# Performance work log

Measured on AMD Instinct MI355X. Metric: run time of the kernel, lower is better.

## Reference

```python
import jax, jax.numpy as jnp
import numpy as np

SEQ = 2048
D_MODEL = 4096
N_HEADS = 16
D_HEAD = D_MODEL // N_HEADS
D_FF = 4 * D_MODEL


def setup_inputs() -> dict:
    key = jax.random.key(0)
    ks = jax.random.split(key, 8)
    s = 0.02
    return {
        "x": jax.random.normal(ks[0], (SEQ, D_MODEL), jnp.float32),
        "attn_bias": jax.random.normal(ks[1], (1, SEQ, SEQ), jnp.float32) * 0.1,
        "ln_scale": jnp.ones((D_MODEL,), jnp.float32),
        "ln_offset": jnp.zeros((D_MODEL,), jnp.float32),
        "wq": jax.random.normal(ks[2], (D_MODEL, D_MODEL), jnp.float32) * s,
        "wk": jax.random.normal(ks[3], (D_MODEL, D_MODEL), jnp.float32) * s,
        "wv": jax.random.normal(ks[4], (D_MODEL, D_MODEL), jnp.float32) * s,
        "wo": jax.random.normal(ks[5], (D_MODEL, D_MODEL), jnp.float32) * s,
        "w_ffn": jax.random.normal(ks[6], (D_MODEL, D_FF), jnp.float32) * s,
        "b_ffn": jnp.zeros((D_FF,), jnp.float32),
        "w_ffn_o": jax.random.normal(ks[7], (D_FF, D_MODEL), jnp.float32) * s,
        "b_ffn_o": jnp.zeros((D_MODEL,), jnp.float32),
    }


def reference(x, attn_bias, ln_scale, ln_offset, wq, wk, wv, wo,
              w_ffn, b_ffn, w_ffn_o, b_ffn_o):
    # ReplicatedLayerNorm (single shard: f_psum is identity)
    mean = jnp.mean(x, axis=-1, keepdims=True)
    var = jnp.var(x, axis=-1, keepdims=True)
    h = ln_scale * jax.lax.rsqrt(var + 1e-5) * (x - mean) + ln_offset

    seq = h.shape[0]
    q = (h @ wq).reshape(seq, N_HEADS, D_HEAD)
    k = (h @ wk).reshape(seq, N_HEADS, D_HEAD)
    v = (h @ wv).reshape(seq, N_HEADS, D_HEAD)

    logits = jnp.einsum('thd,Thd->htT', q, k) / np.float32(np.sqrt(D_HEAD))
    causal = jnp.tril(jnp.ones((seq, seq), jnp.float32))
    logits = logits - 1e10 * (1.0 - causal)
    logits = logits + attn_bias
    weights = jax.nn.softmax(logits, axis=-1)
    attn_vec = jnp.einsum('htT,Thd->thd', weights, v).reshape(seq, D_MODEL)
    attn_out = attn_vec @ wo

    # parallel GELU MLP on the same normed input
    ff = jax.nn.gelu(h @ w_ffn + b_ffn)
    dense_out = ff @ w_ffn_o + b_ffn_o

    return attn_out + dense_out
```

## Files before the change

kernel.cpp:

```cpp
#include <hip/hip_runtime.h>
#include <stdint.h>

#define SEQ 2048
#define DM 4096
#define NHEADS 16
#define DHEAD 256
#define DFF 16384

typedef __attribute__((ext_vector_type(8))) short short8;
typedef __attribute__((ext_vector_type(4))) float f32x4;
typedef __attribute__((ext_vector_type(4))) float float4v;
typedef __attribute__((ext_vector_type(4))) unsigned short ushort4v;
typedef __attribute__((ext_vector_type(8))) unsigned short ushort8v;

__device__ __forceinline__ unsigned short f2b(float f) {
    uint32_t u = __builtin_bit_cast(uint32_t, f);
    u = (u + 0x7FFFu + ((u >> 16) & 1u)) >> 16;
    return (unsigned short)u;
}

__device__ __forceinline__ void gload_lds16(const void* g, void* l) {
    __builtin_amdgcn_global_load_lds((const __attribute__((address_space(1))) void*)g,
                                     (__attribute__((address_space(3))) void*)l, 16, 0, 0);
}

__global__ __launch_bounds__(256) void transpose_all(
    const float* __restrict__ wq, const float* __restrict__ wk, const float* __restrict__ wv,
    const float* __restrict__ wo, const float* __restrict__ wf1, const float* __restrict__ wf2,
    unsigned short* __restrict__ dqkv, unsigned short* __restrict__ dwo,
    unsigned short* __restrict__ df1, unsigned short* __restrict__ df2) {
    int b = blockIdx.x;
    const float* src;
    unsigned short* dst;
    int ldS, ldD, tx;
    if (b < 12288) {
        int w = b >> 12;
        b &= 4095;
        src = (w == 0) ? wq : (w == 1) ? wk : wv;
        dst = dqkv + (size_t)w * DM * DM;
        ldS = DM; ldD = DM; tx = 64;
    } else if (b < 16384) {
        b -= 12288; src = wo; dst = dwo; ldS = DM; ldD = DM; tx = 64;
    } else if (b < 32768) {
        b -= 16384; src = wf1; dst = df1; ldS = DFF; ldD = DM; tx = 256;
    } else {
        b -= 32768; src = wf2; dst = df2; ldS = DM; ldD = DFF; tx = 64;
    }
    const int bx = b % tx, by = b / tx;

    __shared__ unsigned short tl[64 * 66];
    int r0 = by << 6, c0 = bx << 6;
    int tid = threadIdx.x;
#pragma unroll
    for (int it = 0; it < 4; ++it) {
        int e = (tid + it * 256) * 4;
        int rr = e >> 6, cc = e & 63;
        float4v v = *(const float4v*)(src + (size_t)(r0 + rr) * ldS + c0 + cc);
#pragma unroll
        for (int j = 0; j < 4; ++j) tl[rr * 66 + cc + j] = f2b(v[j]);
    }
    __syncthreads();
#pragma unroll
    for (int it = 0; it < 2; ++it) {
        int e = tid + it * 256;
        int oc = e >> 3;
        int k8 = (e & 7) * 8;
        ushort8v w;
#pragma unroll
        for (int j = 0; j < 8; ++j) w[j] = tl[(k8 + j) * 66 + oc];
        *(ushort8v*)(dst + (size_t)(c0 + oc) * ldD + r0 + k8) = w;
    }
}

__global__ __launch_bounds__(256) void transpose_bf(const unsigned short* __restrict__ src,
                                                    unsigned short* __restrict__ dst,
                                                    int ldS, int ldD) {
    __shared__ unsigned short tl[64 * 66];
    int r0 = blockIdx.y << 6, c0 = blockIdx.x << 6;
    int tid = threadIdx.x;
#pragma unroll
    for (int it = 0; it < 4; ++it) {
        int e = (tid + it * 256) * 4;
        int rr = e >> 6, cc = e & 63;
        ushort4v v = *(const ushort4v*)(src + (size_t)(r0 + rr) * ldS + c0 + cc);
#pragma unroll
        for (int j = 0; j < 4; ++j) tl[rr * 66 + cc + j] = v[j];
    }
    __syncthreads();
#pragma unroll
    for (int it = 0; it < 2; ++it) {
        int e = tid + it * 256;
        int oc = e >> 3;
        int k8 = (e & 7) * 8;
        ushort8v w;
#pragma unroll
        for (int j = 0; j < 8; ++j) w[j] = tl[(k8 + j) * 66 + oc];
        *(ushort8v*)(dst + (size_t)(c0 + oc) * ldD + r0 + k8) = w;
    }
}

__global__ __launch_bounds__(256) void ln_kernel(const float* __restrict__ x,
                                                 const float* __restrict__ sc,
                                                 const float* __restrict__ of,
                                                 unsigned short* __restrict__ h) {
    int row = blockIdx.x;
    int tid = threadIdx.x, lane = tid & 63, wave = tid >> 6;
    const float4v* xr = (const float4v*)(x + (size_t)row * DM);
    float4v v[4];
    float s = 0.f, s2 = 0.f;
#pragma unroll
    for (int i = 0; i < 4; ++i) {
        v[i] = xr[tid + i * 256];
#pragma unroll
        for (int j = 0; j < 4; ++j) { s += v[i][j]; s2 += v[i][j] * v[i][j]; }
    }
#pragma unroll
    for (int o = 1; o < 64; o <<= 1) { s += __shfl_xor(s, o); s2 += __shfl_xor(s2, o); }
    __shared__ float rs[4], rs2[4];
    if (lane == 0) { rs[wave] = s; rs2[wave] = s2; }
    __syncthreads();
    s = rs[0] + rs[1] + rs[2] + rs[3];
    s2 = rs2[0] + rs2[1] + rs2[2] + rs2[3];
    float mean = s * (1.0f / DM);
    float var = s2 * (1.0f / DM) - mean * mean;
    float inv = rsqrtf(var + 1e-5f);
#pragma unroll
    for (int i = 0; i < 4; ++i) {
        int c = (tid + i * 256) * 4;
        ushort4v o4;
#pragma unroll
        for (int j = 0; j < 4; ++j)
            o4[j] = f2b((v[i][j] - mean) * inv * sc[c + j] + of[c + j]);
        *(ushort4v*)(h + (size_t)row * DM + c) = o4;
    }
}

#define MF(a, b, c) __builtin_amdgcn_mfma_f32_16x16x32_bf16(a, b, c, 0, 0, 0)
#define FENCE() asm volatile("" ::: "memory")
#define BARR() __builtin_amdgcn_s_barrier()

#define RDA4(BUF, MB)                                                                    \
    _Pragma("unroll") for (int i2 = 0; i2 < 4; ++i2) {                                   \
        af[(MB) + i2][0] = *(const short8*)((BUF) + (arowb + ((MB) + i2) * 16) * 64 + ca0);\
        af[(MB) + i2][1] = *(const short8*)((BUF) + (arowb + ((MB) + i2) * 16) * 64 + ca1);\
    }
#define RDB4(BUF)                                                                        \
    _Pragma("unroll") for (int j2 = 0; j2 < 4; ++j2) {                                   \
        bf[j2][0] = *(const short8*)((BUF) + (brow + j2 * 16) * 64 + ca0);               \
        bf[j2][1] = *(const short8*)((BUF) + (brow + j2 * 16) * 64 + ca1);               \
    }
#define MMQ(MB, NB)                                                                      \
    __builtin_amdgcn_s_setprio(1);                                                       \
    _Pragma("unroll") for (int kk = 0; kk < 2; ++kk)                                     \
        _Pragma("unroll") for (int i2 = 0; i2 < 4; ++i2)                                 \
            _Pragma("unroll") for (int j2 = 0; j2 < 2; ++j2)                             \
                acc[(MB) + i2][(NB) + j2] =                                              \
                    MF(af[(MB) + i2][kk], bf[(NB) + j2][kk], acc[(MB) + i2][(NB) + j2]); \
    __builtin_amdgcn_s_setprio(0)

template <int SPLIT>
__global__ __launch_bounds__(512, 1) void gemm2sq(
    int M, int nwg0,
    const unsigned short* __restrict__ A_0, int K_0, const unsigned short* __restrict__ BT_0,
    void* __restrict__ C_0, int N_0, int ldc_0, const float* __restrict__ bias_0, int epi_0,
    const unsigned short* __restrict__ A_1, int K_1, const unsigned short* __restrict__ BT_1,
    void* __restrict__ C_1, int N_1, int ldc_1, const float* __restrict__ bias_1, int epi_1) {
    __shared__ unsigned short aL[2][256 * 64];
    __shared__ unsigned short bL[2][256 * 64];

    int b = blockIdx.x;
    const unsigned short *A, *BT;
    void* Cout;
    int N, ldc, epi, Kfull;
    const float* bias;
    if (b < nwg0) {
        A = A_0; Kfull = K_0; BT = BT_0; Cout = C_0; N = N_0; ldc = ldc_0; bias = bias_0; epi = epi_0;
    } else {
        b -= nwg0;
        A = A_1; Kfull = K_1; BT = BT_1; Cout = C_1; N = N_1; ldc = ldc_1; bias = bias_1; epi = epi_1;
    }

    const int nby = M >> 8, nbx = N >> 8;
    const int nwg = nby * nbx;
    int sp = 0;
    if (SPLIT == 2) { sp = (b >= nwg) ? 1 : 0; b -= sp * nwg; }
    const int Keff = Kfull / SPLIT;
    const int koff = sp * Keff;

    const int slabw = nbx >> 3;
    const int xcd = b & 7;
    const int jj = b >> 3;
    const int bx = xcd * slabw + jj / nby;
    const int by = jj % nby;
    const int bm0 = by << 8, bn0 = bx << 8;

    const int tid = threadIdx.x, lane = tid & 63, wave = tid >> 6;
    const int wm = wave >> 2, wn = wave & 3;
    const int l15 = lane & 15, kl = lane >> 4;

    const int rh = tid >> 3;
    const int cb_s = (tid & 7) << 4;
    const int kx = (cb_s ^ ((rh & 7) << 4)) >> 1;

    const unsigned short* Abase = A + (size_t)(bm0 + rh) * Kfull + koff + kx;
    const unsigned short* Bbase = BT + (size_t)(bn0 + rh) * Kfull + koff + kx;

    auto stageA = [&](int v, int h) {
        const unsigned short* g = Abase + (size_t)v * 64 + (size_t)(h * 128) * Kfull;
        char* l = (char*)aL[v & 1] + h * 16384 + tid * 16;
        gload_lds16(g, l);
        gload_lds16(g + (size_t)64 * Kfull, l + 8192);
    };
    auto stageB = [&](int v, int h) {
        const unsigned short* g = Bbase + (size_t)v * 64 + (size_t)(h * 128) * Kfull;
        char* l = (char*)bL[v & 1] + h * 16384 + tid * 16;
        gload_lds16(g, l);
        gload_lds16(g + (size_t)64 * Kfull, l + 8192);
    };

    const int arowb = wm * 128 + l15;
    const int brow = wn * 64 + l15;
    const int sa = (l15 & 7) << 4;
    const int ca0 = ((kl * 16) ^ sa) >> 1;
    const int ca1 = ((64 + kl * 16) ^ sa) >> 1;

    f32x4 acc[8][4];
#pragma unroll
    for (int i = 0; i < 8; ++i)
#pragma unroll
        for (int j2 = 0; j2 < 4; ++j2) acc[i][j2] = (f32x4){0.f, 0.f, 0.f, 0.f};

    short8 af[8][2], bf[4][2];

    stageA(0, 0); stageA(0, 1); stageB(0, 0); stageB(0, 1); stageB(1, 0); stageB(1, 1);
    asm volatile("s_waitcnt vmcnt(4)" ::: "memory");
    BARR();

    const int NI = (Keff >> 6) >> 1;
    for (int t2 = 0; t2 < NI; ++t2) {
        const int u = t2 << 1;
        const bool last = (t2 == NI - 1);
        const unsigned short* a0 = aL[0];
        const unsigned short* b0 = bL[0];
        const unsigned short* a1 = aL[1];
        const unsigned short* b1 = bL[1];

        RDA4(a0, 0); RDB4(b0);
        stageA(u + 1, 0);
        FENCE(); BARR();
        MMQ(0, 0);
        BARR();
        RDA4(a0, 4);
        stageA(u + 1, 1);
        FENCE(); BARR();
        MMQ(0, 2);
        BARR();
        if (!last) stageB(u + 2, 0);
        FENCE(); BARR();
        MMQ(4, 0);
        BARR();
        if (!last) stageB(u + 2, 1);
        FENCE(); BARR();
        MMQ(4, 2);
        if (last) { asm volatile("s_waitcnt vmcnt(0)" ::: "memory"); }
        else      { asm volatile("s_waitcnt vmcnt(4)" ::: "memory"); }
        BARR();

        RDA4(a1, 0); RDB4(b1);
        if (!last) stageA(u + 2, 0);
        FENCE(); BARR();
        MMQ(0, 0);
        BARR();
        RDA4(a1, 4);
        if (!last) stageA(u + 2, 1);
        FENCE(); BARR();
        MMQ(0, 2);
        BARR();
        if (!last) stageB(u + 3, 0);
        FENCE(); BARR();
        MMQ(4, 0);
        BARR();
        if (!last) stageB(u + 3, 1);
        FENCE(); BARR();
        MMQ(4, 2);
        if (!last) { asm volatile("s_waitcnt vmcnt(4)" ::: "memory"); }
        BARR();
    }

    const int r0 = bm0 + wm * 128 + kl * 4;
    const int c0g = bn0 + wn * 64 + l15;
#pragma unroll
    for (int mi = 0; mi < 8; ++mi) {
#pragma unroll
        for (int nj = 0; nj < 4; ++nj) {
            int col = c0g + nj * 16;
#pragma unroll
            for (int r = 0; r < 4; ++r) {
                int row = r0 + mi * 16 + r;
                float v = acc[mi][nj][r];
                if (epi == 0) {
                    ((unsigned short*)Cout)[(size_t)row * ldc + col] = f2b(v);
                } else if (epi == 1) {
                    ((float*)Cout)[(size_t)sp * M * N + (size_t)row * ldc + col] = v;
                } else {
                    v += bias[col];
                    float z = 1.5957691216f * (v + 0.044715f * v * v * v);
                    float g = v / (1.0f + __expf(-z));
                    ((unsigned short*)Cout)[(size_t)row * ldc + col] = f2b(g);
                }
            }
        }
    }
}

__global__ __launch_bounds__(256) void final_reduce(const float* __restrict__ fp,
                                                    const float* __restrict__ wp,
                                                    const float* __restrict__ bias,
                                                    float* __restrict__ out) {
    size_t i = (size_t)blockIdx.x * 256 + threadIdx.x;
    const float4v* f0 = (const float4v*)fp;
    const float4v* f1 = (const float4v*)(fp + (size_t)SEQ * DM);
    const float4v* w0 = (const float4v*)wp;
    const float4v* w1 = (const float4v*)(wp + (size_t)SEQ * DM);
    const float4v* b4 = (const float4v*)bias;
    float4v v = f0[i] + f1[i] + w0[i] + w1[i] + b4[i & (DM / 4 - 1)];
    ((float4v*)out)[i] = v;
}

__global__ __launch_bounds__(256, 2) void attn_kernel(const unsigned short* __restrict__ qkv,
                                                      const unsigned short* __restrict__ vT,
                                                      const float* __restrict__ bias,
                                                      unsigned short* __restrict__ attn_vec) {
    __shared__ unsigned short kL[64 * 264];
    __shared__ unsigned short vL[256 * 72];
    __shared__ unsigned short pL[4][16 * 72];

    int qb = blockIdx.x, head = blockIdx.y;
    int tid = threadIdx.x, lane = tid & 63, wave = tid >> 6;
    int q16 = lane & 15, q4 = lane >> 4;

    short8 qf[8];
    {
        const unsigned short* qp =
            qkv + (size_t)(qb * 64 + wave * 16 + q16) * (3 * DM) + head * DHEAD + (q4 << 3);
#pragma unroll
        for (int kk = 0; kk < 8; ++kk) qf[kk] = *(const short8*)(qp + kk * 32);
    }

    f32x4 o[16];
#pragma unroll
    for (int d = 0; d < 16; ++d) o[d] = (f32x4){0.f, 0.f, 0.f, 0.f};
    float m_run[4] = {-INFINITY, -INFINITY, -INFINITY, -INFINITY};
    float l_run[4] = {0.f, 0.f, 0.f, 0.f};
    int qrow0 = qb * 64 + wave * 16 + q4 * 4;

    for (int t = 0; t <= qb; ++t) {
        int kv0 = t * 64;
#pragma unroll
        for (int rr = 0; rr < 8; ++rr) {
            int i = tid + rr * 256;
            int row = i >> 5, c8 = (i & 31) << 3;
            *(ushort8v*)(kL + row * 264 + c8) =
                *(const ushort8v*)(qkv + (size_t)(kv0 + row) * (3 * DM) + DM + head * DHEAD + c8);
        }
#pragma unroll
        for (int rr = 0; rr < 8; ++rr) {
            int i = tid + rr * 256;
            int d = i >> 3, c8 = (i & 7) << 3;
            *(ushort8v*)(vL + d * 72 + c8) =
                *(const ushort8v*)(vT + (size_t)(head * DHEAD + d) * SEQ + kv0 + c8);
        }
        __syncthreads();

        f32x4 s[4];
#pragma unroll
        for (int c = 0; c < 4; ++c) s[c] = (f32x4){0.f, 0.f, 0.f, 0.f};
#pragma unroll
        for (int kk = 0; kk < 8; ++kk) {
#pragma unroll
            for (int c = 0; c < 4; ++c) {
                short8 kf = *(const short8*)(kL + (c * 16 + q16) * 264 + kk * 32 + (q4 << 3));
                s[c] = __builtin_amdgcn_mfma_f32_16x16x32_bf16(qf[kk], kf, s[c], 0, 0, 0);
            }
        }

        bool diag = (t == qb);
#pragma unroll
        for (int r = 0; r < 4; ++r) {
            int qr = qrow0 + r;
            float sv[4];
#pragma unroll
            for (int c = 0; c < 4; ++c) {
                float vv = s[c][r] * 0.0625f + bias[(size_t)qr * SEQ + kv0 + c * 16 + q16];
                if (diag && (kv0 + c * 16 + q16) > qr) vv = -1e30f;
                sv[c] = vv;
            }
            float m = fmaxf(fmaxf(sv[0], sv[1]), fmaxf(sv[2], sv[3]));
#pragma unroll
            for (int off = 1; off < 16; off <<= 1) m = fmaxf(m, __shfl_xor(m, off));
            float mn = fmaxf(m_run[r], m);
            float alpha = __expf(m_run[r] - mn);
            float psum = 0.f;
#pragma unroll
            for (int c = 0; c < 4; ++c) {
                float p = __expf(sv[c] - mn);
                psum += p;
                pL[wave][(q4 * 4 + r) * 72 + c * 16 + q16] = f2b(p);
            }
#pragma unroll
            for (int off = 1; off < 16; off <<= 1) psum += __shfl_xor(psum, off);
            l_run[r] = l_run[r] * alpha + psum;
            m_run[r] = mn;
#pragma unroll
            for (int d = 0; d < 16; ++d) o[d][r] *= alpha;
        }

#pragma unroll
        for (int ks = 0; ks < 2; ++ks) {
            short8 pa = *(const short8*)(pL[wave] + q16 * 72 + ks * 32 + (q4 << 3));
#pragma unroll
            for (int d = 0; d < 16; ++d) {
                short8 vb = *(const short8*)(vL + (d * 16 + q16) * 72 + ks * 32 + (q4 << 3));
                o[d] = __builtin_amdgcn_mfma_f32_16x16x32_bf16(pa, vb, o[d], 0, 0, 0);
            }
        }
        __syncthreads();
    }

#pragma unroll
    for (int r = 0; r < 4; ++r) {
        float inv = 1.0f / l_run[r];
#pragma unroll
        for (int d = 0; d < 16; ++d)
            attn_vec[(size_t)(qrow0 + r) * DM + head * DHEAD + d * 16 + q16] = f2b(o[d][r] * inv);
    }
}

extern "C" void kernel_launch(void* const* d_in, const int* in_sizes, int n_in,
                              void* d_out, int out_size, void* d_ws, size_t ws_size,
                              hipStream_t stream) {
    const float* x = (const float*)d_in[0];
    const float* attn_bias = (const float*)d_in[1];
    const float* ln_scale = (const float*)d_in[2];
    const float* ln_offset = (const float*)d_in[3];
    const float* wq = (const float*)d_in[4];
    const float* wk = (const float*)d_in[5];
    const float* wv = (const float*)d_in[6];
    const float* wo = (const float*)d_in[7];
    const float* w_ffn = (const float*)d_in[8];
    const float* b_ffn = (const float*)d_in[9];
    const float* w_ffn_o = (const float*)d_in[10];
    const float* b_ffn_o = (const float*)d_in[11];
    float* out = (float*)d_out;

    char* p = (char*)d_ws;
    unsigned short* WT_qkv = (unsigned short*)p; p += (size_t)3 * DM * DM * 2;
    unsigned short* WT_o = (unsigned short*)p;   p += (size_t)DM * DM * 2;
    unsigned short* WT_f1 = (unsigned short*)p;  p += (size_t)DFF * DM * 2;
    unsigned short* WT_f2 = (unsigned short*)p;  p += (size_t)DM * DFF * 2;
    unsigned short* hB = (unsigned short*)p;     p += (size_t)SEQ * DM * 2;
    unsigned short* qkvB = (unsigned short*)p;   p += (size_t)SEQ * 3 * DM * 2;
    unsigned short* vTB = (unsigned short*)p;    p += (size_t)DM * SEQ * 2;
    unsigned short* avB = (unsigned short*)p;    p += (size_t)SEQ * DM * 2;
    unsigned short* ffB = (unsigned short*)p;    p += (size_t)SEQ * DFF * 2;

    float* fp = (float*)WT_qkv;
    float* wp = (float*)WT_f1;

    transpose_all<<<49152, 256, 0, stream>>>(wq, wk, wv, wo, w_ffn, w_ffn_o,
                                             WT_qkv, WT_o, WT_f1, WT_f2);

    ln_kernel<<<SEQ, 256, 0, stream>>>(x, ln_scale, ln_offset, hB);

    gemm2sq<1><<<896, 512, 0, stream>>>(
        SEQ, 384,
        hB, DM, WT_qkv, qkvB, 3 * DM, 3 * DM, nullptr, 0,
        hB, DM, WT_f1, ffB, DFF, DFF, b_ffn, 2);

    transpose_bf<<<dim3(DM / 64, SEQ / 64), 256, 0, stream>>>(qkvB + 2 * DM, vTB, 3 * DM, SEQ);

    attn_kernel<<<dim3(SEQ / 64, NHEADS), 256, 0, stream>>>(qkvB, vTB, attn_bias, avB);

    gemm2sq<2><<<512, 512, 0, stream>>>(
        SEQ, 256,
        avB, DM, WT_o, wp, DM, DM, nullptr, 1,
        ffB, DFF, WT_f2, fp, DM, DM, nullptr, 1);

    final_reduce<<<(SEQ * DM / 4) / 256, 256, 0, stream>>>(fp, wp, b_ffn_o, out);
}
```

Baseline: 1.243 ms.

## Overlap weight transposes with LayerNorm and attention, drop extra GEMM barriers

LayerNorm is folded into a combined pre-kernel together with the QKV and FFN1 weight transposes. The Wo and FFN2 weight transposes are moved into extra blocks of the attention kernel. Those transposes can then use CUs left idle by the 512 attention blocks, instead of running as a separate serial pass before everything else. Separately, the compiler fences and barriers placed before each MFMA quarter in the GEMM main loop are removed to cut synchronisation. This adds a risk of LDS read/write races if those barriers guarded buffer reuse. It also makes the shared-memory use and register pressure of the fused kernels heavier.

Measured after the change: 1.447 ms. 1.16x slower.

```diff
diff --git a/kernel.cpp b/kernel.cpp
--- a/kernel.cpp
+++ b/kernel.cpp
@@ -24,12 +24,75 @@
                                      (__attribute__((address_space(3))) void*)l, 16, 0, 0);
 }
 
-__global__ __launch_bounds__(256) void transpose_all(
+__device__ __forceinline__ void transpose_tile_f32(const float* __restrict__ src,
+                                                   unsigned short* __restrict__ dst,
+                                                   int ldS, int ldD, int bx, int by,
+                                                   unsigned short* tl) {
+    int r0 = by << 6, c0 = bx << 6;
+    int tid = threadIdx.x;
+#pragma unroll
+    for (int it = 0; it < 4; ++it) {
+        int e = (tid + it * 256) * 4;
+        int rr = e >> 6, cc = e & 63;
+        float4v v = *(const float4v*)(src + (size_t)(r0 + rr) * ldS + c0 + cc);
+#pragma unroll
+        for (int j = 0; j < 4; ++j) tl[rr * 66 + cc + j] = f2b(v[j]);
+    }
+    __syncthreads();
+#pragma unroll
+    for (int it = 0; it < 2; ++it) {
+        int e = tid + it * 256;
+        int oc = e >> 3;
+        int k8 = (e & 7) * 8;
+        ushort8v w;
+#pragma unroll
+        for (int j = 0; j < 8; ++j) w[j] = tl[(k8 + j) * 66 + oc];
+        *(ushort8v*)(dst + (size_t)(c0 + oc) * ldD + r0 + k8) = w;
+    }
+}
+
+__global__ __launch_bounds__(256) void pre_kernel(
+    const float* __restrict__ x, const float* __restrict__ sc, const float* __restrict__ of,
+    unsigned short* __restrict__ h,
     const float* __restrict__ wq, const float* __restrict__ wk, const float* __restrict__ wv,
-    const float* __restrict__ wo, const float* __restrict__ wf1, const float* __restrict__ wf2,
-    unsigned short* __restrict__ dqkv, unsigned short* __restrict__ dwo,
-    unsigned short* __restrict__ df1, unsigned short* __restrict__ df2) {
+    const float* __restrict__ wf1,
+    unsigned short* __restrict__ dqkv, unsigned short* __restrict__ df1) {
+    __shared__ unsigned short tl[64 * 66];
+    __shared__ float rs[4], rs2[4];
     int b = blockIdx.x;
+    if (b < SEQ) {
+        int row = b;
+        int tid = threadIdx.x, lane = tid & 63, wave = tid >> 6;
+        const float4v* xr = (const float4v*)(x + (size_t)row * DM);
+        float4v v[4];
+        float s = 0.f, s2 = 0.f;
+#pragma unroll
+        for (int i = 0; i < 4; ++i) {
+            v[i] = xr[tid + i * 256];
+#pragma unroll
+            for (int j = 0; j < 4; ++j) { s += v[i][j]; s2 += v[i][j] * v[i][j]; }
+        }
+#pragma unroll
+        for (int o = 1; o < 64; o <<= 1) { s += __shfl_xor(s, o); s2 += __shfl_xor(s2, o); }
+        if (lane == 0) { rs[wave] = s; rs2[wave] = s2; }
+        __syncthreads();
+        s = rs[0] + rs[1] + rs[2] + rs[3];
+        s2 = rs2[0] + rs2[1] + rs2[2] + rs2[3];
+        float mean = s * (1.0f / DM);
+        float var = s2 * (1.0f / DM) - mean * mean;
+        float inv = rsqrtf(var + 1e-5f);
+#pragma unroll
+        for (int i = 0; i < 4; ++i) {
+            int c = (tid + i * 256) * 4;
+            ushort4v o4;
+#pragma unroll
+            for (int j = 0; j < 4; ++j)
+                o4[j] = f2b((v[i][j] - mean) * inv * sc[c + j] + of[c + j]);
+            *(ushort4v*)(h + (size_t)row * DM + c) = o4;
+        }
+        return;
+    }
+    b -= SEQ;
     const float* src;
     unsigned short* dst;
     int ldS, ldD, tx;
@@ -39,37 +102,10 @@
         src = (w == 0) ? wq : (w == 1) ? wk : wv;
         dst = dqkv + (size_t)w * DM * DM;
         ldS = DM; ldD = DM; tx = 64;
-    } else if (b < 16384) {
-        b -= 12288; src = wo; dst = dwo; ldS = DM; ldD = DM; tx = 64;
-    } else if (b < 32768) {
-        b -= 16384; src = wf1; dst = df1; ldS = DFF; ldD = DM; tx = 256;
     } else {
-        b -= 32768; src = wf2; dst = df2; ldS = DM; ldD = DFF; tx = 64;
-    }
-    const int bx = b % tx, by = b / tx;
-
-    __shared__ unsigned short tl[64 * 66];
-    int r0 = by << 6, c0 = bx << 6;
-    int tid = threadIdx.x;
-#pragma unroll
-    for (int it = 0; it < 4; ++it) {
-        int e = (tid + it * 256) * 4;
-        int rr = e >> 6, cc = e & 63;
-        float4v v = *(const float4v*)(src + (size_t)(r0 + rr) * ldS + c0 + cc);
-#pragma unroll
-        for (int j = 0; j < 4; ++j) tl[rr * 66 + cc + j] = f2b(v[j]);
-    }
-    __syncthreads();
-#pragma unroll
-    for (int it = 0; it < 2; ++it) {
-        int e = tid + it * 256;
-        int oc = e >> 3;
-        int k8 = (e & 7) * 8;
-        ushort8v w;
-#pragma unroll
-        for (int j = 0; j < 8; ++j) w[j] = tl[(k8 + j) * 66 + oc];
-        *(ushort8v*)(dst + (size_t)(c0 + oc) * ldD + r0 + k8) = w;
-    }
+        b -= 12288; src = wf1; dst = df1; ldS = DFF; ldD = DM; tx = 256;
+    }
+    transpose_tile_f32(src, dst, ldS, ldD, b % tx, b / tx, tl);
 }
 
 __global__ __launch_bounds__(256) void transpose_bf(const unsigned short* __restrict__ src,
@@ -99,44 +135,7 @@
     }
 }
 
-__global__ __launch_bounds__(256) void ln_kernel(const float* __restrict__ x,
-                                                 const float* __restrict__ sc,
-                                                 const float* __restrict__ of,
-                                                 unsigned short* __restrict__ h) {
-    int row = blockIdx.x;
-    int tid = threadIdx.x, lane = tid & 63, wave = tid >> 6;
-    const float4v* xr = (const float4v*)(x + (size_t)row * DM);
-    float4v v[4];
-    float s = 0.f, s2 = 0.f;
-#pragma unroll
-    for (int i = 0; i < 4; ++i) {
-        v[i] = xr[tid + i * 256];
-#pragma unroll
-        for (int j = 0; j < 4; ++j) { s += v[i][j]; s2 += v[i][j] * v[i][j]; }
-    }
-#pragma unroll
-    for (int o = 1; o < 64; o <<= 1) { s += __shfl_xor(s, o); s2 += __shfl_xor(s2, o); }
-    __shared__ float rs[4], rs2[4];
-    if (lane == 0) { rs[wave] = s; rs2[wave] = s2; }
-    __syncthreads();
-    s = rs[0] + rs[1] + rs[2] + rs[3];
-    s2 = rs2[0] + rs2[1] + rs2[2] + rs2[3];
-    float mean = s * (1.0f / DM);
-    float var = s2 * (1.0f / DM) - mean * mean;
-    float inv = rsqrtf(var + 1e-5f);
-#pragma unroll
-    for (int i = 0; i < 4; ++i) {
-        int c = (tid + i * 256) * 4;
-        ushort4v o4;
-#pragma unroll
-        for (int j = 0; j < 4; ++j)
-            o4[j] = f2b((v[i][j] - mean) * inv * sc[c + j] + of[c + j]);
-        *(ushort4v*)(h + (size_t)row * DM + c) = o4;
-    }
-}
-
 #define MF(a, b, c) __builtin_amdgcn_mfma_f32_16x16x32_bf16(a, b, c, 0, 0, 0)
-#define FENCE() asm volatile("" ::: "memory")
 #define BARR() __builtin_amdgcn_s_barrier()
 
 #define RDA4(BUF, MB)                                                                    \
@@ -247,20 +246,16 @@
 
         RDA4(a0, 0); RDB4(b0);
         stageA(u + 1, 0);
-        FENCE(); BARR();
         MMQ(0, 0);
         BARR();
         RDA4(a0, 4);
         stageA(u + 1, 1);
-        FENCE(); BARR();
         MMQ(0, 2);
         BARR();
         if (!last) stageB(u + 2, 0);
-        FENCE(); BARR();
         MMQ(4, 0);
         BARR();
         if (!last) stageB(u + 2, 1);
-        FENCE(); BARR();
         MMQ(4, 2);
         if (last) { asm volatile("s_waitcnt vmcnt(0)" ::: "memory"); }
         else      { asm volatile("s_waitcnt vmcnt(4)" ::: "memory"); }
@@ -268,20 +263,16 @@
 
         RDA4(a1, 0); RDB4(b1);
         if (!last) stageA(u + 2, 0);
-        FENCE(); BARR();
         MMQ(0, 0);
         BARR();
         RDA4(a1, 4);
         if (!last) stageA(u + 2, 1);
-        FENCE(); BARR();
         MMQ(0, 2);
         BARR();
         if (!last) stageB(u + 3, 0);
-        FENCE(); BARR();
         MMQ(4, 0);
         BARR();
         if (!last) stageB(u + 3, 1);
-        FENCE(); BARR();
         MMQ(4, 2);
         if (!last) { asm volatile("s_waitcnt vmcnt(4)" ::: "memory"); }
         BARR();
@@ -327,15 +318,31 @@
     ((float4v*)out)[i] = v;
 }
 
-__global__ __launch_bounds__(256, 2) void attn_kernel(const unsigned short* __restrict__ qkv,
-                                                      const unsigned short* __restrict__ vT,
-                                                      const float* __restrict__ bias,
-                                                      unsigned short* __restrict__ attn_vec) {
-    __shared__ unsigned short kL[64 * 264];
-    __shared__ unsigned short vL[256 * 72];
-    __shared__ unsigned short pL[4][16 * 72];
-
-    int qb = blockIdx.x, head = blockIdx.y;
+__global__ __launch_bounds__(256, 2) void attn_plus(const unsigned short* __restrict__ qkv,
+                                                    const unsigned short* __restrict__ vT,
+                                                    const float* __restrict__ bias,
+                                                    unsigned short* __restrict__ attn_vec,
+                                                    const float* __restrict__ wo,
+                                                    const float* __restrict__ wf2,
+                                                    unsigned short* __restrict__ dwo,
+                                                    unsigned short* __restrict__ df2) {
+    __shared__ unsigned short sm[64 * 264 + 256 * 72 + 4 * 16 * 72];
+    int bb = blockIdx.x;
+    if (bb >= 512) {
+        bb -= 512;
+        const float* src;
+        unsigned short* dst;
+        int ldS, ldD;
+        if (bb < 4096) { src = wo; dst = dwo; ldS = DM; ldD = DM; }
+        else { bb -= 4096; src = wf2; dst = df2; ldS = DM; ldD = DFF; }
+        transpose_tile_f32(src, dst, ldS, ldD, bb % 64, bb / 64, sm);
+        return;
+    }
+    unsigned short* kL = sm;
+    unsigned short* vL = sm + 64 * 264;
+    unsigned short* pL = vL + 256 * 72;
+
+    int qb = bb & 31, head = bb >> 5;
     int tid = threadIdx.x, lane = tid & 63, wave = tid >> 6;
     int q16 = lane & 15, q4 = lane >> 4;
 
@@ -405,7 +412,7 @@
             for (int c = 0; c < 4; ++c) {
                 float p = __expf(sv[c] - mn);
                 psum += p;
-                pL[wave][(q4 * 4 + r) * 72 + c * 16 + q16] = f2b(p);
+                pL[wave * (16 * 72) + (q4 * 4 + r) * 72 + c * 16 + q16] = f2b(p);
             }
 #pragma unroll
             for (int off = 1; off < 16; off <<= 1) psum += __shfl_xor(psum, off);
@@ -417,7 +424,7 @@
 
 #pragma unroll
         for (int ks = 0; ks < 2; ++ks) {
-            short8 pa = *(const short8*)(pL[wave] + q16 * 72 + ks * 32 + (q4 << 3));
+            short8 pa = *(const short8*)(pL + wave * (16 * 72) + q16 * 72 + ks * 32 + (q4 << 3));
 #pragma unroll
             for (int d = 0; d < 16; ++d) {
                 short8 vb = *(const short8*)(vL + (d * 16 + q16) * 72 + ks * 32 + (q4 << 3));
@@ -467,10 +474,8 @@
     float* fp = (float*)WT_qkv;
     float* wp = (float*)WT_f1;
 
-    transpose_all<<<49152, 256, 0, stream>>>(wq, wk, wv, wo, w_ffn, w_ffn_o,
-                                             WT_qkv, WT_o, WT_f1, WT_f2);
-
-    ln_kernel<<<SEQ, 256, 0, stream>>>(x, ln_scale, ln_offset, hB);
+    pre_kernel<<<30720, 256, 0, stream>>>(x, ln_scale, ln_offset, hB,
+                                          wq, wk, wv, w_ffn, WT_qkv, WT_f1);
 
     gemm2sq<1><<<896, 512, 0, stream>>>(
         SEQ, 384,
@@ -479,7 +484,8 @@
 
     transpose_bf<<<dim3(DM / 64, SEQ / 64), 256, 0, stream>>>(qkvB + 2 * DM, vTB, 3 * DM, SEQ);
 
-    attn_kernel<<<dim3(SEQ / 64, NHEADS), 256, 0, stream>>>(qkvB, vTB, attn_bias, avB);
+    attn_plus<<<20992, 256, 0, stream>>>(qkvB, vTB, attn_bias, avB,
+                                         wo, w_ffn_o, WT_o, WT_f2);
 
     gemm2sq<2><<<512, 512, 0, stream>>>(
         SEQ, 256,
```
